# Kernel optimization log

Measured on AMD Instinct MI355X. Metric: run time of the kernel, lower is better.

## Reference

```python
import jax, jax.numpy as jnp
import numpy as np

B, P, ENC, DEC, EMB, ATT, FFN, V, MAXLEN = 64, 196, 512, 512, 256, 128, 1024, 2000, 160
T = MAXLEN - 1
EPS = 1e-5

def _k(i):
    return jax.random.fold_in(jax.random.key(0), i)

def _w(i, shape):
    return jax.random.normal(_k(i), shape, jnp.float32) * 0.02

def setup_inputs() -> dict:
    lens = jnp.concatenate([jnp.array([MAXLEN]), jax.random.randint(_k(2), (B - 1,), 2, MAXLEN + 1)])
    return {
        "encoder_out": jax.random.normal(_k(0), (B, P, ENC), jnp.float32),
        "encoded_captions": jax.random.randint(_k(1), (B, MAXLEN), 0, V),
        "caption_lengths": lens,
        "enc_att_w": _w(3, (ATT, ENC)), "enc_att_b": _w(4, (ATT,)),
        "dec_att_w": _w(5, (ATT, DEC)), "dec_att_b": _w(6, (ATT,)),
        "full_att_w": _w(7, (1, ATT)), "full_att_b": _w(8, (1,)),
        "gate_w1": _w(9, (ATT, DEC)), "gate_b1": _w(10, (ATT,)),
        "gate_w2": _w(11, (1, ATT)), "gate_b2": _w(12, (1,)),
        "emb": jax.random.uniform(_k(13), (V, EMB), jnp.float32, -0.1, 0.1),
        "gru1_wih": _w(14, (3 * DEC, EMB + ENC)), "gru1_whh": _w(15, (3 * DEC, DEC)),
        "gru1_bih": _w(16, (3 * DEC,)), "gru1_bhh": _w(17, (3 * DEC,)),
        "gru2_wih": _w(18, (3 * DEC, DEC)), "gru2_whh": _w(19, (3 * DEC, DEC)),
        "gru2_bih": _w(20, (3 * DEC,)), "gru2_bhh": _w(21, (3 * DEC,)),
        "proj_w": _w(22, (DEC, EMB + ENC)), "proj_b": _w(23, (DEC,)),
        "ln1_g": jnp.ones((DEC,), jnp.float32), "ln1_b": jnp.zeros((DEC,), jnp.float32),
        "ln2_g": jnp.ones((DEC,), jnp.float32), "ln2_b": jnp.zeros((DEC,), jnp.float32),
        "ffn_w1": _w(24, (FFN, DEC)), "ffn_b1": jnp.zeros((FFN,), jnp.float32),
        "ffn_w2": _w(25, (V, FFN)), "ffn_b2": jnp.zeros((V,), jnp.float32),
    }

def _gru(x, h, wih, whh, bih, bhh):
    gi = x @ wih.T + bih
    gh = h @ whh.T + bhh
    ir, iz, ig = jnp.split(gi, 3, axis=-1)
    hr, hz, hg = jnp.split(gh, 3, axis=-1)
    r = jax.nn.sigmoid(ir + hr)
    z = jax.nn.sigmoid(iz + hz)
    n = jnp.tanh(ig + r * hg)
    return (1.0 - z) * n + z * h

def _ln(x, g, b):
    m = x.mean(-1, keepdims=True)
    v = x.var(-1, keepdims=True)
    return (x - m) / jnp.sqrt(v + EPS) * g + b

def _decode(encoder_out, encoded_captions, caption_lengths,
            enc_att_w, enc_att_b, dec_att_w, dec_att_b, full_att_w, full_att_b,
            gate_w1, gate_b1, gate_w2, gate_b2, emb,
            gru1_wih, gru1_whh, gru1_bih, gru1_bhh,
            gru2_wih, gru2_whh, gru2_bih, gru2_bhh,
            proj_w, proj_b, ln1_g, ln1_b, ln2_g, ln2_b,
            ffn_w1, ffn_b1, ffn_w2, ffn_b2):
    # sort by caption length descending (packed-sequence style)
    order = jnp.argsort(-caption_lengths)
    enc = encoder_out[order]                       # [B,P,ENC]
    caps = encoded_captions[order]                 # [B,MAXLEN]
    dec_lens = caption_lengths[order] - 1          # [B]
    att1 = enc @ enc_att_w.T + enc_att_b           # [B,P,ATT] (loop-invariant)
    xs = jnp.swapaxes(emb[caps[:, :T]], 0, 1)      # [T,B,EMB] teacher forcing (p=1.0)
    masks = (jnp.arange(T)[:, None] < dec_lens[None, :]).astype(enc.dtype)  # [T,B]

    def step(carry, inp):
        h1, h2 = carry
        x_t, m = inp                               # [B,EMB], [B]
        att2 = h2 @ dec_att_w.T + dec_att_b        # [B,ATT]
        e = (jax.nn.relu(att1 + att2[:, None, :]) @ full_att_w.T + full_att_b)[..., 0]  # [B,P]
        alpha = jax.nn.softmax(e, axis=1)
        awe = jnp.einsum('bpe,bp->be', enc, alpha)
        gate = jax.nn.sigmoid(jax.nn.relu(h2 @ gate_w1.T + gate_b1) @ gate_w2.T + gate_b2)  # [B,1]
        awe = awe * gate
        gin = jnp.concatenate([x_t, awe], axis=1)  # [B,EMB+ENC]
        h1_new = _gru(gin, h1, gru1_wih, gru1_whh, gru1_bih, gru1_bhh)
        h1_res = _ln(h1_new + gin @ proj_w.T + proj_b, ln1_g, ln1_b)
        h2_new = _gru(h1_res, h2, gru2_wih, gru2_whh, gru2_bih, gru2_bhh)
        h2_res = _ln(h2_new + h1_res, ln2_g, ln2_b)  # dropout is identity (eval)
        preds = jax.nn.relu(h2_res @ ffn_w1.T + ffn_b1) @ ffn_w2.T + ffn_b2  # [B,V]
        mc = m[:, None]
        h1 = jnp.where(mc > 0, h1_new, h1)
        h2 = jnp.where(mc > 0, h2_new, h2)
        return (h1, h2), (preds * mc, alpha * mc)

    h0 = jnp.zeros((enc.shape[0], DEC), enc.dtype)
    _, (preds, alphas) = jax.lax.scan(step, (h0, h0), (xs, masks))
    predictions = jnp.swapaxes(preds, 0, 1)        # [B,T,V]
    alphas = jnp.swapaxes(alphas, 0, 1)            # [B,T,P]
    return predictions, caps, dec_lens, alphas, order

def reference(encoder_out, encoded_captions, caption_lengths,
              enc_att_w, enc_att_b, dec_att_w, dec_att_b, full_att_w, full_att_b,
              gate_w1, gate_b1, gate_w2, gate_b2, emb,
              gru1_wih, gru1_whh, gru1_bih, gru1_bhh,
              gru2_wih, gru2_whh, gru2_bih, gru2_bhh,
              proj_w, proj_b, ln1_g, ln1_b, ln2_g, ln2_b,
              ffn_w1, ffn_b1, ffn_w2, ffn_b2):
    return _decode(encoder_out, encoded_captions, caption_lengths,
                   enc_att_w, enc_att_b, dec_att_w, dec_att_b, full_att_w, full_att_b,
                   gate_w1, gate_b1, gate_w2, gate_b2, emb,
                   gru1_wih, gru1_whh, gru1_bih, gru1_bhh,
                   gru2_wih, gru2_whh, gru2_bih, gru2_bhh,
                   proj_w, proj_b, ln1_g, ln1_b, ln2_g, ln2_b,
                   ffn_w1, ffn_b1, ffn_w2, ffn_b2)
```

## Files before the change

### kernel.cpp

```cpp
#include <hip/hip_runtime.h>
#include <math.h>

#define B 64
#define P 196
#define ENCD 512
#define DECD 512
#define EMBD 256
#define ATTD 128
#define FFND 1024
#define VV 2000
#define MAXLEN 160
#define TSTEPS 159
#define EPS 1e-5f

#define OUT_PRED ((size_t)0)
#define OUT_CAPS ((size_t)(B * TSTEPS * VV))
#define OUT_DECL (OUT_CAPS + (size_t)(B * MAXLEN))
#define OUT_ALPH (OUT_DECL + (size_t)B)
#define OUT_ORDR (OUT_ALPH + (size_t)(B * TSTEPS * P))


struct Ctx {
  const float* enc; const int* caps_in; const int* lens_in;
  const float* eaw; const float* eab; const float* daw; const float* dab;
  const float* faw; const float* fab;
  const float* gw1; const float* gb1; const float* gw2; const float* gb2;
  const float* emb;
  const float* wih1; const float* whh1; const float* bih1; const float* bhh1;
  const float* wih2; const float* whh2; const float* bih2; const float* bhh2;
  const float* projw; const float* projb;
  const float* ln1g; const float* ln1b; const float* ln2g; const float* ln2b;
  const float* fw1; const float* fb1; const float* fw2; const float* fb2;
  int* leafs; int* root;
  int* order_i; int* declen; int* caps_s;
  float* EaT; float* att1;
  float* h1; float* h2; float* v1; float* v2;
  float* gin; float* fgr; float* gh1g; float* gh2g; float* att2acc;
  float* stats1; float* stats2;
  float* WA; float* WB; float* WC; float* WD; float* Watt;
  float* Sf; float* cbf; float* Sg; float* cbg;
  float* out;
};

__device__ __forceinline__ float sigf(float x) { return 1.f / (1.f + __expf(-x)); }

__device__ __forceinline__ float ld4(const float* p) {
  unsigned int u = __hip_atomic_load((const unsigned int*)p, __ATOMIC_RELAXED, __HIP_MEMORY_SCOPE_AGENT);
  return __uint_as_float(u);
}
__device__ __forceinline__ void st4(float* p, float v) {
  __hip_atomic_store((unsigned int*)p, __float_as_uint(v), __ATOMIC_RELAXED, __HIP_MEMORY_SCOPE_AGENT);
}
__device__ __forceinline__ void st8(float* p, float a, float b2) {
  unsigned long long v = ((unsigned long long)__float_as_uint(b2) << 32) | (unsigned long long)__float_as_uint(a);
  __hip_atomic_store((unsigned long long*)p, v, __ATOMIC_RELAXED, __HIP_MEMORY_SCOPE_AGENT);
}
__device__ __forceinline__ void atomF(float* p, float v) {
  __hip_atomic_fetch_add(p, v, __ATOMIC_RELAXED, __HIP_MEMORY_SCOPE_AGENT);
}
__device__ __forceinline__ float4 ldg16(const float* p) {
  float4 d;
  asm volatile("global_load_dwordx4 %0, %1, off sc0 sc1" : "=v"(d) : "v"(p));
  return d;
}
__device__ __forceinline__ void vmwait() { asm volatile("s_waitcnt vmcnt(0)" ::: "memory"); }

__device__ __forceinline__ unsigned short tobf(float x) {
  unsigned int u = __float_as_uint(x);
  u += 0x7fffu + ((u >> 16) & 1u);
  return (unsigned short)(u >> 16);
}
__device__ __forceinline__ float frombf(unsigned short s) {
  return __uint_as_float(((unsigned int)s) << 16);
}


__global__ void k_order(Ctx c) {
  __shared__ int lens[B];
  int tid = threadIdx.x;
  lens[tid] = c.lens_in[tid];
  __syncthreads();
  int li = lens[tid];
  int pos = 0;
  for (int j = 0; j < B; ++j) {
    int lj = lens[j];
    pos += (lj > li || (lj == li && j < tid)) ? 1 : 0;
  }
  c.order_i[pos] = tid;
  c.declen[pos] = li - 1;
  c.out[OUT_ORDR + pos] = (float)tid;
  c.out[OUT_DECL + pos] = (float)(li - 1);
}

__global__ __launch_bounds__(256) void k_caps(Ctx c) {
  int idx = blockIdx.x * 256 + threadIdx.x;
  if (idx < B * MAXLEN) {
    int b = idx / MAXLEN, t = idx - b * MAXLEN;
    int v = c.caps_in[c.order_i[b] * MAXLEN + t];
    c.caps_s[idx] = v;
    c.out[OUT_CAPS + idx] = (float)v;
  }
}

__global__ __launch_bounds__(256) void k_eat(Ctx c) {
  int idx = blockIdx.x * 256 + threadIdx.x;
  if (idx < 128 * 512) {
    int k = idx >> 7, d = idx & 127;
    c.EaT[(size_t)k * 128 + d] = c.eaw[(size_t)d * 512 + k];
  }
}

__global__ __launch_bounds__(256) void k_att1(Ctx c) {
  __shared__ float Xs[8 * 512];
  int tid = threadIdx.x;
  int r0 = blockIdx.x * 8;
  for (int idx = tid; idx < 8 * 512; idx += 256) {
    int rr = idx >> 9, k = idx & 511;
    int r = r0 + rr;
    int b = r / P, p = r - b * P;
    int ob = c.order_i[b];
    Xs[idx] = c.enc[((size_t)(ob * P + p)) * ENCD + k];
  }
  __syncthreads();
  int d = tid >> 1, kh = tid & 1;
  float acc[8];
#pragma unroll
  for (int rr = 0; rr < 8; ++rr) acc[rr] = 0.f;
  int kbase = kh * 256;
  for (int k = 0; k < 256; ++k) {
    float w = c.EaT[(size_t)(kbase + k) * 128 + d];
#pragma unroll
    for (int rr = 0; rr < 8; ++rr) acc[rr] = fmaf(w, Xs[rr * 512 + kbase + k], acc[rr]);
  }
#pragma unroll
  for (int rr = 0; rr < 8; ++rr) {
    acc[rr] += __shfl_xor(acc[rr], 1);
    if (kh == 0) c.att1[(size_t)(r0 + rr) * 128 + d] = acc[rr];
  }
}

__global__ __launch_bounds__(256) void k_wpa(Ctx c) {
  int s = blockIdx.x;
  float* dst = c.WA + (size_t)s * 65536;
  for (int idx = threadIdx.x; idx < 65536; idx += 256) {
    int kb = idx >> 9, r = idx & 511, cc = r >> 2, jj = r & 3;
    int col = s * 128 + cc, k = kb * 4 + jj;
    float v;
    if (col < 1536) v = c.whh1[(size_t)col * 512 + k];
    else if (col < 3072) v = c.whh2[(size_t)(col - 1536) * 512 + k];
    else v = c.ln2g[k] * c.fw1[(size_t)(col - 3072) * 512 + k];
    dst[idx] = v;
  }
}

__global__ __launch_bounds__(256) void k_wpb(Ctx c) {
  int s = blockIdx.x;
  float* dst = c.WB + (size_t)s * 49152;
  for (int idx = threadIdx.x; idx < 49152; idx += 256) {
    int kb = idx >> 8, r = idx & 255, cc = r >> 2, jj = r & 3;
    int u = s * 64 + cc, k = kb * 4 + jj;
    int d = u >> 2, comp = u & 3;
    dst[idx] = (comp < 3) ? c.wih1[(size_t)(comp * 512 + d) * 768 + k]
                          : c.projw[(size_t)d * 768 + k];
  }
}

__global__ __launch_bounds__(256) void k_wpc(Ctx c) {
  int s = blockIdx.x;
  float* dst = c.WC + (size_t)s * 24576;
  for (int idx = threadIdx.x; idx < 24576; idx += 256) {
    int kb = idx / 192, r = idx - kb * 192, cc = r >> 2, jj = r & 3;
    int u = s * 48 + cc, k = kb * 4 + jj;
    int d = u / 3, comp = u - d * 3;
    dst[idx] = c.ln1g[k] * c.wih2[(size_t)(comp * 512 + d) * 512 + k];
  }
}

__global__ __launch_bounds__(256) void k_wpd(Ctx c) {
  int s = blockIdx.x;
  float* dst = c.WD + (size_t)s * 65536;
  for (int idx = threadIdx.x; idx < 65536; idx += 256) {
    int kb = idx >> 8, r = idx & 255, cc = r >> 2, jj = r & 3;
    int vcol = s * 64 + cc, k = kb * 4 + jj;
    dst[idx] = (vcol < 2000) ? c.fw2[(size_t)vcol * 1024 + k] : 0.f;
  }
}

__global__ __launch_bounds__(256) void k_watt(Ctx c) {
  int ks = blockIdx.x;
  float* dst = c.Watt + (size_t)ks * 16384;
  for (int idx = threadIdx.x; idx < 16384; idx += 256) {
    int kb = idx >> 10, r = idx & 1023, cc = r >> 2, jj = r & 3;
    int k = ks * 64 + kb * 4 + jj;
    dst[idx] = (cc < 128) ? c.daw[(size_t)cc * 512 + k] : c.gw1[(size_t)(cc - 128) * 512 + k];
  }
}

__global__ __launch_bounds__(256) void k_consts(Ctx c) {
  __shared__ float r1[256], r2[256];
  int i = blockIdx.x, tid = threadIdx.x;
  float a = 0.f, b2 = 0.f;
  if (i < 1024) {
    const float* w = c.fw1 + (size_t)i * 512;
    for (int k = tid; k < 512; k += 256) { a = fmaf(c.ln2g[k], w[k], a); b2 = fmaf(c.ln2b[k], w[k], b2); }
  } else {
    const float* w = c.wih2 + (size_t)(i - 1024) * 512;
    for (int k = tid; k < 512; k += 256) { a = fmaf(c.ln1g[k], w[k], a); b2 = fmaf(c.ln1b[k], w[k], b2); }
  }
  r1[tid] = a; r2[tid] = b2;
  __syncthreads();
  for (int s = 128; s > 0; s >>= 1) {
    if (tid < s) { r1[tid] += r1[tid + s]; r2[tid] += r2[tid + s]; }
    __syncthreads();
  }
  if (tid == 0) {
    if (i < 1024) { c.Sf[i] = r1[0]; c.cbf[i] = r2[0] + c.fb1[i]; }
    else { c.Sg[i - 1024] = r1[0]; c.cbg[i - 1024] = r2[0] + c.bih2[i - 1024]; }
  }
}


__device__ __forceinline__ void gridbar(int* leafs, int* root, int ph) {
  __builtin_amdgcn_s_waitcnt(0);
  __syncthreads();
  if (threadIdx.x == 0) {
    int old = __hip_atomic_fetch_add(&leafs[(blockIdx.x & 7) * 32], 1,
                                     __ATOMIC_RELAXED, __HIP_MEMORY_SCOPE_AGENT);
    if (old == ph * 32 - 1)
      __hip_atomic_fetch_add(root, 1, __ATOMIC_RELAXED, __HIP_MEMORY_SCOPE_AGENT);
    while (__hip_atomic_load(root, __ATOMIC_RELAXED, __HIP_MEMORY_SCOPE_AGENT) < ph * 8)
      __builtin_amdgcn_s_sleep(1);
  }
  __syncthreads();
}

__global__ __launch_bounds__(512) void persist(Ctx c) {
  __shared__ unsigned short att1L[196 * 130];
  __shared__ unsigned short encL[196 * 128];
  __shared__ float SH[12288];
  __shared__ float eL[256];
  __shared__ float alphaL[256];
  __shared__ float redS[256];
  __shared__ float att2sL[128], fawL[128], dabL[128], gb1L[128];
  __shared__ float sstat[16];
  __shared__ int declenI[64];
  __shared__ float gateL, gb2v, fabv;

  const int g = blockIdx.x;
  const int tid = threadIdx.x;
  const int cg = g & 31;
  const int rg = g >> 5;
  const int r0 = rg * 8;
  const int bA = g >> 2, q = g & 3;
  const int kc = tid >> 6;
  const int ct = tid & 63;

  if (tid < 128) {
    fawL[tid] = c.faw[tid];
    dabL[tid] = c.dab[tid] + c.eab[tid];
    gb1L[tid] = c.gb1[tid];
  }
  if (tid == 0) { gb2v = c.gb2[0]; fabv = c.fab[0]; }
  if (tid < 64) declenI[tid] = c.declen[tid];
  {
    const int ob = c.order_i[bA];
    for (int idx = tid; idx < 196 * 128; idx += 512) {
      int p = idx >> 7, j = idx & 127;
      att1L[p * 130 + j] = tobf(c.att1[((size_t)bA * P + p) * 128 + j]);
      encL[idx] = tobf(c.enc[((size_t)(ob * P + p)) * 512 + q * 128 + j]);
    }
  }
  __syncthreads();

  int ph = 0;
  for (int t = 0; t < MAXLEN; ++t) {
    {
      float* XS = SH;
      float* RED = SH + 4096;
      const float* hsrc = ((cg < 12) ? c.h1 : (cg < 24) ? c.h2 : c.v2) + (size_t)r0 * 512;
      float4 s0 = ldg16(hsrc + tid * 4);
      float4 s1 = ldg16(hsrc + 2048 + tid * 4);
      if (tid < 8) {
        int slot = (t + 1) & 1;
        float a = ld4(c.stats2 + slot * 128 + (r0 + tid) * 2);
        float b2 = ld4(c.stats2 + slot * 128 + (r0 + tid) * 2 + 1);
        float m = a * (1.f / 512.f);
        float va = b2 * (1.f / 512.f) - m * m;
        sstat[tid] = m; sstat[8 + tid] = rsqrtf(va + EPS);
      }
      vmwait();
      *(float4*)(XS + tid * 4) = s0;
      *(float4*)(XS + 2048 + tid * 4) = s1;
      __syncthreads();

      {
        const float* wp = c.WA + (size_t)cg * 65536 + kc * 8192 + ct * 4;
        const float* xb = XS + kc * 64;
        float acc[8][2];
#pragma unroll
        for (int r = 0; r < 8; ++r) { acc[r][0] = 0.f; acc[r][1] = 0.f; }
#pragma unroll 4
        for (int i = 0; i < 16; ++i) {
          float4 w0 = *(const float4*)(wp + i * 512);
          float4 w1 = *(const float4*)(wp + i * 512 + 256);
#pragma unroll
          for (int r = 0; r < 8; ++r) {
            float4 x = *(const float4*)(xb + r * 512 + i * 4);
            acc[r][0] = fmaf(w0.x, x.x, fmaf(w0.y, x.y, fmaf(w0.z, x.z, fmaf(w0.w, x.w, acc[r][0]))));
            acc[r][1] = fmaf(w1.x, x.x, fmaf(w1.y, x.y, fmaf(w1.z, x.z, fmaf(w1.w, x.w, acc[r][1]))));
          }
        }
#pragma unroll
        for (int r = 0; r < 8; ++r) {
          RED[(kc * 8 + r) * 128 + ct] = acc[r][0];
          RED[(kc * 8 + r) * 128 + ct + 64] = acc[r][1];
        }
      }
      if (cg >= 16 && cg < 24) {
        const int ks_att = cg - 16;
        const int ct2 = tid >> 1, half = tid & 1;
        const float* wp = c.Watt + (size_t)ks_att * 16384 + half * 8192 + ct2 * 4;
        const float* xb = XS + ks_att * 64 + half * 32;
        float a[8];
#pragma unroll
        for (int r = 0; r < 8; ++r) a[r] = 0.f;
#pragma unroll
        for (int i = 0; i < 8; ++i) {
          float4 w = *(const float4*)(wp + i * 1024);
#pragma unroll
          for (int r = 0; r < 8; ++r) {
            float4 x = *(const float4*)(xb + r * 512 + i * 4);
            a[r] = fmaf(w.x, x.x, fmaf(w.y, x.y, fmaf(w.z, x.z, fmaf(w.w, x.w, a[r]))));
          }
        }
#pragma unroll
        for (int r = 0; r < 8; ++r) {
          a[r] += __shfl_xor(a[r], 1);
          if (half == 0) atomF(c.att2acc + (r0 + r) * 256 + ct2, a[r]);
        }
      }
      __syncthreads();
      {
        int row = tid >> 6, cp = (tid & 63) * 2;
        float s0_ = 0.f, s1_ = 0.f;
#pragma unroll
        for (int k8 = 0; k8 < 8; ++k8) {
          float2 v = *(const float2*)(RED + (k8 * 8 + row) * 128 + cp);
          s0_ += v.x; s1_ += v.y;
        }
        int bb = r0 + row;
        int gcol = cg * 128 + cp;
        if (cg < 12) st8(c.gh1g + bb * 1536 + gcol, s0_, s1_);
        else if (cg < 24) st8(c.gh2g + bb * 1536 + (gcol - 1536), s0_, s1_);
        else {
          int cf = gcol - 3072;
          float m2 = sstat[row], i2 = sstat[8 + row];
          float v0 = i2 * (s0_ - m2 * c.Sf[cf]) + c.cbf[cf];
          float v1v = i2 * (s1_ - m2 * c.Sf[cf + 1]) + c.cbf[cf + 1];
          st8(c.fgr + bb * 1024 + cf, fmaxf(v0, 0.f), fmaxf(v1v, 0.f));
        }
      }
    }
    gridbar(c.leafs, c.root, ++ph);

    {
      float* XS = SH;
      float* RED = SH + 8192;
      const float* fsrc = c.fgr + (size_t)r0 * 1024;
      float4 s0 = ldg16(fsrc + tid * 4);
      float4 s1 = ldg16(fsrc + 2048 + tid * 4);
      float4 s2 = ldg16(fsrc + 4096 + tid * 4);
      float4 s3 = ldg16(fsrc + 6144 + tid * 4);
      if (g == 0) {
        int sl = t & 1;
        if (tid < 128) st4(c.stats1 + sl * 128 + tid, 0.f);
        else if (tid < 256) st4(c.stats2 + sl * 128 + (tid - 128), 0.f);
      }
      vmwait();
      *(float4*)(XS + tid * 4) = s0;
      *(float4*)(XS + 2048 + tid * 4) = s1;
      *(float4*)(XS + 4096 + tid * 4) = s2;
      *(float4*)(XS + 6144 + tid * 4) = s3;
      __syncthreads();

      {
        const float* wp = c.WD + (size_t)cg * 65536 + kc * 8192 + ct * 4;
        const float* xb = XS + kc * 128;
        float acc[8];
#pragma unroll
        for (int r = 0; r < 8; ++r) acc[r] = 0.f;
#pragma unroll 4
        for (int i = 0; i < 32; ++i) {
          float4 w = *(const float4*)(wp + i * 256);
#pragma unroll
          for (int r = 0; r < 8; ++r) {
            float4 x = *(const float4*)(xb + r * 1024 + i * 4);
            acc[r] = fmaf(w.x, x.x, fmaf(w.y, x.y, fmaf(w.z, x.z, fmaf(w.w, x.w, acc[r]))));
          }
        }
#pragma unroll
        for (int r = 0; r < 8; ++r) RED[(kc * 8 + r) * 64 + ct] = acc[r];
      }
      __syncthreads();
      {
        int row = tid >> 6, cl = tid & 63;
        float s = 0.f;
#pragma unroll
        for (int k8 = 0; k8 < 8; ++k8) s += RED[(k8 * 8 + row) * 64 + cl];
        int bb = r0 + row, vcol = cg * 64 + cl;
        if (vcol < 2000 && t > 0 && (t - 1) < declenI[bb])
          c.out[OUT_PRED + ((size_t)bb * TSTEPS + (t - 1)) * VV + vcol] = s + c.fb2[vcol];
      }
      if (tid < 128) {
        att2sL[tid] = ld4(c.att2acc + bA * 256 + tid) + dabL[tid];
        float g1 = fmaxf(ld4(c.att2acc + bA * 256 + 128 + tid) + gb1L[tid], 0.f);
        redS[tid] = g1 * c.gw2[tid];
      } else if (tid < 256) redS[tid] = 0.f;
      __syncthreads();
      for (int s2_ = 64; s2_ > 0; s2_ >>= 1) {
        if (tid < s2_) redS[tid] += redS[tid + s2_];
        __syncthreads();
      }
      if (tid == 0) gateL = sigf(redS[0] + gb2v);
      __syncthreads();
      {
        int p = tid >> 1, jh = tid & 1;
        float e = 0.f;
        if (p < 196) {
          const unsigned short* ap = att1L + p * 130 + jh * 64;
#pragma unroll 8
          for (int j = 0; j < 64; ++j)
            e = fmaf(fmaxf(frombf(ap[j]) + att2sL[jh * 64 + j], 0.f), fawL[jh * 64 + j], e);
        }
        e += __shfl_xor(e, 1);
        if (jh == 0 && p < 196) eL[p] = e + fabv;
      }
      __syncthreads();
      if (tid < 256) redS[tid] = (tid < 196) ? eL[tid] : -3.0e38f;
      __syncthreads();
      for (int s2_ = 128; s2_ > 0; s2_ >>= 1) {
        if (tid < s2_) redS[tid] = fmaxf(redS[tid], redS[tid + s2_]);
        __syncthreads();
      }
      float mx = redS[0];
      __syncthreads();
      float ex = (tid < 196) ? __expf(eL[tid] - mx) : 0.f;
      if (tid < 256) redS[tid] = ex;
      __syncthreads();
      for (int s2_ = 128; s2_ > 0; s2_ >>= 1) {
        if (tid < s2_) redS[tid] += redS[tid + s2_];
        __syncthreads();
      }
      float inv = 1.f / redS[0];
      if (tid < 256) alphaL[tid] = ex * inv;
      if (q == 0 && tid < 196 && t < declenI[bA])
        c.out[OUT_ALPH + ((size_t)bA * TSTEPS + t) * P + tid] = ex * inv;
      __syncthreads();
      {
        int el = tid & 127, pq = tid >> 7;
        const unsigned short* ep2 = encL + (size_t)(pq * 49) * 128 + el;
        const float* alp = alphaL + pq * 49;
        float s_ = 0.f;
#pragma unroll
        for (int i = 0; i < 49; ++i) s_ = fmaf(alp[i], frombf(ep2[(size_t)i * 128]), s_);
        RED[tid] = s_;
      }
      __syncthreads();
      if (tid < 128) {
        float aw = RED[tid] + RED[128 + tid] + RED[256 + tid] + RED[384 + tid];
        st4(c.gin + bA * 768 + 256 + q * 128 + tid, aw * gateL);
      }
      if (q == 1 && tid < 256) {
        int tok = c.caps_s[bA * MAXLEN + t];
        st4(c.gin + bA * 768 + tid, c.emb[(size_t)tok * 256 + tid]);
      }
    }
    gridbar(c.leafs, c.root, ++ph);

    {
      float* XS = SH;
      float* RED = SH + 6144;
      const float* gsrc = c.gin + (size_t)r0 * 768;
      float4 s0 = ldg16(gsrc + tid * 4);
      float4 s1 = ldg16(gsrc + 2048 + tid * 4);
      float4 s2 = ldg16(gsrc + 4096 + tid * 4);
      if (g < 32) st4(c.att2acc + g * 512 + tid, 0.f);
      vmwait();
      *(float4*)(XS + tid * 4) = s0;
      *(float4*)(XS + 2048 + tid * 4) = s1;
      *(float4*)(XS + 4096 + tid * 4) = s2;
      __syncthreads();

      {
        const float* wp = c.WB + (size_t)cg * 49152 + kc * 6144 + ct * 4;
        const float* xb = XS + kc * 96;
        float acc[8];
#pragma unroll
        for (int r = 0; r < 8; ++r) acc[r] = 0.f;
#pragma unroll 4
        for (int i = 0; i < 24; ++i) {
          float4 w = *(const float4*)(wp + i * 256);
#pragma unroll
          for (int r = 0; r < 8; ++r) {
            float4 x = *(const float4*)(xb + r * 768 + i * 4);
            acc[r] = fmaf(w.x, x.x, fmaf(w.y, x.y, fmaf(w.z, x.z, fmaf(w.w, x.w, acc[r]))));
          }
        }
#pragma unroll
        for (int r = 0; r < 8; ++r) RED[(kc * 8 + r) * 64 + ct] = acc[r];
      }
      __syncthreads();
      if (tid < 128) {
        int row = tid >> 4, dl = tid & 15;
        int bb = r0 + row, d = cg * 16 + dl;
        float gi0 = 0.f, gi1 = 0.f, gi2v = 0.f, gi3 = 0.f;
#pragma unroll
        for (int k8 = 0; k8 < 8; ++k8) {
          float4 v = *(const float4*)(RED + (k8 * 8 + row) * 64 + dl * 4);
          gi0 += v.x; gi1 += v.y; gi2v += v.z; gi3 += v.w;
        }
        float gir = gi0 + c.bih1[d];
        float giz = gi1 + c.bih1[512 + d];
        float gig = gi2v + c.bih1[1024 + d];
        float pj = gi3 + c.projb[d];
        float hr = ld4(c.gh1g + bb * 1536 + d) + c.bhh1[d];
        float hz = ld4(c.gh1g + bb * 1536 + 512 + d) + c.bhh1[512 + d];
        float hg = ld4(c.gh1g + bb * 1536 + 1024 + d) + c.bhh1[1024 + d];
        float r_ = sigf(gir + hr);
        float z_ = sigf(giz + hz);
        float n_ = tanhf(gig + r_ * hg);
        float hold = ld4(c.h1 + bb * 512 + d);
        float hnew = (1.f - z_) * n_ + z_ * hold;
        st4(c.h1 + bb * 512 + d, (t < declenI[bb]) ? hnew : hold);
        float v1v = hnew + pj;
        st4(c.v1 + bb * 512 + d, v1v);
        float ss = v1v, sq = v1v * v1v;
#pragma unroll
        for (int w = 1; w < 16; w <<= 1) { ss += __shfl_xor(ss, w); sq += __shfl_xor(sq, w); }
        if (dl == 0) {
          atomF(c.stats1 + (t & 1) * 128 + bb * 2, ss);
          atomF(c.stats1 + (t & 1) * 128 + bb * 2 + 1, sq);
        }
      }
    }
    gridbar(c.leafs, c.root, ++ph);

    {
      float* XS = SH;
      float* RED = SH + 4096;
      const float* vsrc = c.v1 + (size_t)r0 * 512;
      float4 s0 = ldg16(vsrc + tid * 4);
      float4 s1 = ldg16(vsrc + 2048 + tid * 4);
      if (tid < 8) {
        float a = ld4(c.stats1 + (t & 1) * 128 + (r0 + tid) * 2);
        float b2 = ld4(c.stats1 + (t & 1) * 128 + (r0 + tid) * 2 + 1);
        float m = a * (1.f / 512.f);
        float va = b2 * (1.f / 512.f) - m * m;
        sstat[tid] = m; sstat[8 + tid] = rsqrtf(va + EPS);
      }
      vmwait();
      *(float4*)(XS + tid * 4) = s0;
      *(float4*)(XS + 2048 + tid * 4) = s1;
      __syncthreads();

      if (ct < 48) {
        const float* wp = c.WC + (size_t)cg * 24576 + kc * 3072 + ct * 4;
        const float* xb = XS + kc * 64;
        float acc[8];
#pragma unroll
        for (int r = 0; r < 8; ++r) acc[r] = 0.f;
#pragma unroll 4
        for (int i = 0; i < 16; ++i) {
          float4 w = *(const float4*)(wp + i * 192);
#pragma unroll
          for (int r = 0; r < 8; ++r) {
            float4 x = *(const float4*)(xb + r * 512 + i * 4);
            acc[r] = fmaf(w.x, x.x, fmaf(w.y, x.y, fmaf(w.z, x.z, fmaf(w.w, x.w, acc[r]))));
          }
        }
#pragma unroll
        for (int r = 0; r < 8; ++r) RED[(kc * 8 + r) * 48 + ct] = acc[r];
      }
      __syncthreads();
      if (tid < 128) {
        int row = tid >> 4, dl = tid & 15;
        int bb = r0 + row, d = cg * 16 + dl;
        float gi0 = 0.f, gi1 = 0.f, gi2v = 0.f;
#pragma unroll
        for (int k8 = 0; k8 < 8; ++k8) {
          const float* rp = RED + (k8 * 8 + row) * 48 + dl * 3;
          gi0 += rp[0]; gi1 += rp[1]; gi2v += rp[2];
        }
        float m1 = sstat[row], i1 = sstat[8 + row];
        float gir = i1 * (gi0 - m1 * c.Sg[d]) + c.cbg[d];
        float giz = i1 * (gi1 - m1 * c.Sg[512 + d]) + c.cbg[512 + d];
        float gig = i1 * (gi2v - m1 * c.Sg[1024 + d]) + c.cbg[1024 + d];
        float hr = ld4(c.gh2g + bb * 1536 + d) + c.bhh2[d];
        float hz = ld4(c.gh2g + bb * 1536 + 512 + d) + c.bhh2[512 + d];
        float hg = ld4(c.gh2g + bb * 1536 + 1024 + d) + c.bhh2[1024 + d];
        float r_ = sigf(gir + hr);
        float z_ = sigf(giz + hz);
        float n_ = tanhf(gig + r_ * hg);
        float hold = ld4(c.h2 + bb * 512 + d);
        float hnew = (1.f - z_) * n_ + z_ * hold;
        st4(c.h2 + bb * 512 + d, (t < declenI[bb]) ? hnew : hold);
        float h1r = (XS[row * 512 + d] - m1) * i1 * c.ln1g[d] + c.ln1b[d];
        float v2v = hnew + h1r;
        st4(c.v2 + bb * 512 + d, v2v);
        float ss = v2v, sq = v2v * v2v;
#pragma unroll
        for (int w = 1; w < 16; w <<= 1) { ss += __shfl_xor(ss, w); sq += __shfl_xor(sq, w); }
        if (dl == 0) {
          atomF(c.stats2 + (t & 1) * 128 + bb * 2, ss);
          atomF(c.stats2 + (t & 1) * 128 + bb * 2 + 1, sq);
        }
      }
    }
    gridbar(c.leafs, c.root, ++ph);
  }
}

extern "C" void kernel_launch(void* const* d_in, const int* in_sizes, int n_in,
                              void* d_out, int out_size, void* d_ws, size_t ws_size,
                              hipStream_t stream) {
  (void)in_sizes; (void)n_in; (void)ws_size;
  Ctx c;
  c.enc = (const float*)d_in[0];
  c.caps_in = (const int*)d_in[1];
  c.lens_in = (const int*)d_in[2];
  c.eaw = (const float*)d_in[3];
  c.eab = (const float*)d_in[4];
  c.daw = (const float*)d_in[5];
  c.dab = (const float*)d_in[6];
  c.faw = (const float*)d_in[7];
  c.fab = (const float*)d_in[8];
  c.gw1 = (const float*)d_in[9];
  c.gb1 = (const float*)d_in[10];
  c.gw2 = (const float*)d_in[11];
  c.gb2 = (const float*)d_in[12];
  c.emb = (const float*)d_in[13];
  c.wih1 = (const float*)d_in[14];
  c.whh1 = (const float*)d_in[15];
  c.bih1 = (const float*)d_in[16];
  c.bhh1 = (const float*)d_in[17];
  c.wih2 = (const float*)d_in[18];
  c.whh2 = (const float*)d_in[19];
  c.bih2 = (const float*)d_in[20];
  c.bhh2 = (const float*)d_in[21];
  c.projw = (const float*)d_in[22];
  c.projb = (const float*)d_in[23];
  c.ln1g = (const float*)d_in[24];
  c.ln1b = (const float*)d_in[25];
  c.ln2g = (const float*)d_in[26];
  c.ln2b = (const float*)d_in[27];
  c.fw1 = (const float*)d_in[28];
  c.fb1 = (const float*)d_in[29];
  c.fw2 = (const float*)d_in[30];
  c.fb2 = (const float*)d_in[31];
  c.out = (float*)d_out;

  char* wp_ = (char*)d_ws;
  auto alloc = [&](size_t bytes) -> char* {
    char* p = wp_;
    wp_ += (bytes + 255) & ~(size_t)255;
    return p;
  };
  char* zbase = wp_;
  c.leafs = (int*)alloc(256 * 4);
  c.root = (int*)alloc(256);
  c.h1 = (float*)alloc((size_t)B * 512 * 4);
  c.h2 = (float*)alloc((size_t)B * 512 * 4);
  c.stats1 = (float*)alloc(2 * 64 * 2 * 4);
  c.stats2 = (float*)alloc(2 * 64 * 2 * 4);
  c.att2acc = (float*)alloc((size_t)B * 256 * 4);
  c.v2 = (float*)alloc((size_t)B * 512 * 4);
  size_t zbytes = (size_t)(wp_ - zbase);

  c.order_i = (int*)alloc(B * 4);
  c.declen = (int*)alloc(B * 4);
  c.caps_s = (int*)alloc((size_t)B * MAXLEN * 4);
  c.EaT = (float*)alloc((size_t)512 * 128 * 4);
  c.att1 = (float*)alloc((size_t)B * P * 128 * 4);
  c.v1 = (float*)alloc((size_t)B * 512 * 4);
  c.gin = (float*)alloc((size_t)B * 768 * 4);
  c.fgr = (float*)alloc((size_t)B * 1024 * 4);
  c.gh1g = (float*)alloc((size_t)B * 1536 * 4);
  c.gh2g = (float*)alloc((size_t)B * 1536 * 4);
  c.WA = (float*)alloc((size_t)32 * 65536 * 4);
  c.WB = (float*)alloc((size_t)32 * 49152 * 4);
  c.WC = (float*)alloc((size_t)32 * 24576 * 4);
  c.WD = (float*)alloc((size_t)32 * 65536 * 4);
  c.Watt = (float*)alloc((size_t)8 * 16384 * 4);
  c.Sf = (float*)alloc(1024 * 4);
  c.cbf = (float*)alloc(1024 * 4);
  c.Sg = (float*)alloc(1536 * 4);
  c.cbg = (float*)alloc(1536 * 4);

  hipMemsetAsync(d_out, 0, (size_t)out_size * 4, stream);
  hipMemsetAsync(zbase, 0, zbytes, stream);

  k_order<<<1, 64, 0, stream>>>(c);
  k_caps<<<(B * MAXLEN + 255) / 256, 256, 0, stream>>>(c);
  k_eat<<<(128 * 512 + 255) / 256, 256, 0, stream>>>(c);
  k_att1<<<(B * P) / 8, 256, 0, stream>>>(c);
  k_wpa<<<32, 256, 0, stream>>>(c);
  k_wpb<<<32, 256, 0, stream>>>(c);
  k_wpc<<<32, 256, 0, stream>>>(c);
  k_wpd<<<32, 256, 0, stream>>>(c);
  k_watt<<<8, 256, 0, stream>>>(c);
  k_consts<<<2560, 256, 0, stream>>>(c);

  persist<<<256, 512, 0, stream>>>(c);
}
```

Measured before the change: 13.97 ms.

## Prefetch next-phase weights before grid barriers and use wave-shuffle reductions

At the end of each phase of the persistent kernel, each thread issues dummy global loads covering the weight slice the next phase will read. The intent is to warm L2/MALL during the grid barrier so the next GEMV does not stall on cold weight fetches. It also replaces the tree-based shared-memory reductions for the gate, softmax max and softmax sum with wave-level shuffle reductions, cutting many __syncthreads. The gate inputs are now loaded early, alongside the fgr loads. The cost is extra memory traffic and register pressure, and the sink asm forces each phase to wait for the prefetch loads to complete.

Result: slower. 14.38 ms (+3.0%).

```diff
diff --git a/kernel.cpp b/kernel.cpp
--- a/kernel.cpp
+++ b/kernel.cpp
@@ -65,6 +65,19 @@
 }
 __device__ __forceinline__ void vmwait() { asm volatile("s_waitcnt vmcnt(0)" ::: "memory"); }
 
+__device__ __forceinline__ float pfl(const float* p) {
+  float v;
+  asm volatile("global_load_dword %0, %1, off" : "=v"(v) : "v"(p));
+  return v;
+}
+__device__ __forceinline__ void pfsink8(float a, float b, float c2, float d,
+                                        float e, float f, float g2, float h) {
+  asm volatile("" :: "v"(a), "v"(b), "v"(c2), "v"(d), "v"(e), "v"(f), "v"(g2), "v"(h));
+}
+__device__ __forceinline__ void pfsink2(float a, float b) {
+  asm volatile("" :: "v"(a), "v"(b));
+}
+
 __device__ __forceinline__ unsigned short tobf(float x) {
   unsigned int u = __float_as_uint(x);
   u += 0x7fffu + ((u >> 16) & 1u);
@@ -240,11 +253,11 @@
   __shared__ float SH[12288];
   __shared__ float eL[256];
   __shared__ float alphaL[256];
-  __shared__ float redS[256];
-  __shared__ float att2sL[128], fawL[128], dabL[128], gb1L[128];
+  __shared__ float att2sL[128], fawL[128], dabL[128], gb1L[128], gw2L[128];
+  __shared__ float wred[16];
   __shared__ float sstat[16];
   __shared__ int declenI[64];
-  __shared__ float gateL, gb2v, fabv;
+  __shared__ float gb2v, fabv;
 
   const int g = blockIdx.x;
   const int tid = threadIdx.x;
@@ -259,6 +272,7 @@
     fawL[tid] = c.faw[tid];
     dabL[tid] = c.dab[tid] + c.eab[tid];
     gb1L[tid] = c.gb1[tid];
+    gw2L[tid] = c.gw2[tid];
   }
   if (tid == 0) { gb2v = c.gb2[0]; fabv = c.fab[0]; }
   if (tid < 64) declenI[tid] = c.declen[tid];
@@ -339,6 +353,12 @@
           if (half == 0) atomF(c.att2acc + (r0 + r) * 256 + ct2, a[r]);
         }
       }
+      float pw[8];
+      {
+        const float* pb = c.WD + (size_t)cg * 65536 + tid * 16;
+#pragma unroll
+        for (int i = 0; i < 8; ++i) pw[i] = pfl(pb + i * 8192);
+      }
       __syncthreads();
       {
         int row = tid >> 6, cp = (tid & 63) * 2;
@@ -360,6 +380,7 @@
           st8(c.fgr + bb * 1024 + cf, fmaxf(v0, 0.f), fmaxf(v1v, 0.f));
         }
       }
+      pfsink8(pw[0], pw[1], pw[2], pw[3], pw[4], pw[5], pw[6], pw[7]);
     }
     gridbar(c.leafs, c.root, ++ph);
 
@@ -371,6 +392,11 @@
       float4 s1 = ldg16(fsrc + 2048 + tid * 4);
       float4 s2 = ldg16(fsrc + 4096 + tid * 4);
       float4 s3 = ldg16(fsrc + 6144 + tid * 4);
+      float a2r = 0.f, g1r = 0.f;
+      if (tid < 128) {
+        a2r = ld4(c.att2acc + bA * 256 + tid);
+        g1r = ld4(c.att2acc + bA * 256 + 128 + tid);
+      }
       if (g == 0) {
         int sl = t & 1;
         if (tid < 128) st4(c.stats1 + sl * 128 + tid, 0.f);
@@ -381,6 +407,14 @@
       *(float4*)(XS + 2048 + tid * 4) = s1;
       *(float4*)(XS + 4096 + tid * 4) = s2;
       *(float4*)(XS + 6144 + tid * 4) = s3;
+      if (tid < 128) {
+        att2sL[tid] = a2r + dabL[tid];
+        float g1 = fmaxf(g1r + gb1L[tid], 0.f);
+        float gv = g1 * gw2L[tid];
+#pragma unroll
+        for (int w = 1; w < 64; w <<= 1) gv += __shfl_xor(gv, w);
+        if ((tid & 63) == 0) wred[tid >> 6] = gv;
+      }
       __syncthreads();
 
       {
@@ -401,6 +435,12 @@
 #pragma unroll
         for (int r = 0; r < 8; ++r) RED[(kc * 8 + r) * 64 + ct] = acc[r];
       }
+      float pw[6];
+      {
+        const float* pb = c.WB + (size_t)cg * 49152 + tid * 16;
+#pragma unroll
+        for (int i = 0; i < 6; ++i) pw[i] = pfl(pb + i * 8192);
+      }
       __syncthreads();
       {
         int row = tid >> 6, cl = tid & 63;
@@ -411,18 +451,6 @@
         if (vcol < 2000 && t > 0 && (t - 1) < declenI[bb])
           c.out[OUT_PRED + ((size_t)bb * TSTEPS + (t - 1)) * VV + vcol] = s + c.fb2[vcol];
       }
-      if (tid < 128) {
-        att2sL[tid] = ld4(c.att2acc + bA * 256 + tid) + dabL[tid];
-        float g1 = fmaxf(ld4(c.att2acc + bA * 256 + 128 + tid) + gb1L[tid], 0.f);
-        redS[tid] = g1 * c.gw2[tid];
-      } else if (tid < 256) redS[tid] = 0.f;
-      __syncthreads();
-      for (int s2_ = 64; s2_ > 0; s2_ >>= 1) {
-        if (tid < s2_) redS[tid] += redS[tid + s2_];
-        __syncthreads();
-      }
-      if (tid == 0) gateL = sigf(redS[0] + gb2v);
-      __syncthreads();
       {
         int p = tid >> 1, jh = tid & 1;
         float e = 0.f;
@@ -436,22 +464,25 @@
         if (jh == 0 && p < 196) eL[p] = e + fabv;
       }
       __syncthreads();
-      if (tid < 256) redS[tid] = (tid < 196) ? eL[tid] : -3.0e38f;
-      __syncthreads();
-      for (int s2_ = 128; s2_ > 0; s2_ >>= 1) {
-        if (tid < s2_) redS[tid] = fmaxf(redS[tid], redS[tid + s2_]);
-        __syncthreads();
-      }
-      float mx = redS[0];
-      __syncthreads();
-      float ex = (tid < 196) ? __expf(eL[tid] - mx) : 0.f;
-      if (tid < 256) redS[tid] = ex;
-      __syncthreads();
-      for (int s2_ = 128; s2_ > 0; s2_ >>= 1) {
-        if (tid < s2_) redS[tid] += redS[tid + s2_];
-        __syncthreads();
-      }
-      float inv = 1.f / redS[0];
+      float ev = (tid < 196) ? eL[tid] : -3.0e38f;
+      if (tid < 256) {
+        float mv = ev;
+#pragma unroll
+        for (int w = 1; w < 64; w <<= 1) mv = fmaxf(mv, __shfl_xor(mv, w));
+        if ((tid & 63) == 0) wred[2 + (tid >> 6)] = mv;
+      }
+      __syncthreads();
+      float mx = fmaxf(fmaxf(wred[2], wred[3]), fmaxf(wred[4], wred[5]));
+      float ex = (tid < 196) ? __expf(ev - mx) : 0.f;
+      if (tid < 256) {
+        float sv = ex;
+#pragma unroll
+        for (int w = 1; w < 64; w <<= 1) sv += __shfl_xor(sv, w);
+        if ((tid & 63) == 0) wred[6 + (tid >> 6)] = sv;
+      }
+      __syncthreads();
+      float inv = 1.f / (wred[6] + wred[7] + wred[8] + wred[9]);
+      float gate = sigf(wred[0] + wred[1] + gb2v);
       if (tid < 256) alphaL[tid] = ex * inv;
       if (q == 0 && tid < 196 && t < declenI[bA])
         c.out[OUT_ALPH + ((size_t)bA * TSTEPS + t) * P + tid] = ex * inv;
@@ -468,12 +499,13 @@
       __syncthreads();
       if (tid < 128) {
         float aw = RED[tid] + RED[128 + tid] + RED[256 + tid] + RED[384 + tid];
-        st4(c.gin + bA * 768 + 256 + q * 128 + tid, aw * gateL);
+        st4(c.gin + bA * 768 + 256 + q * 128 + tid, aw * gate);
       }
       if (q == 1 && tid < 256) {
         int tok = c.caps_s[bA * MAXLEN + t];
         st4(c.gin + bA * 768 + tid, c.emb[(size_t)tok * 256 + tid]);
       }
+      pfsink8(pw[0], pw[1], pw[2], pw[3], pw[4], pw[5], pw[0], pw[1]);
     }
     gridbar(c.leafs, c.root, ++ph);
 
@@ -508,6 +540,12 @@
         }
 #pragma unroll
         for (int r = 0; r < 8; ++r) RED[(kc * 8 + r) * 64 + ct] = acc[r];
+      }
+      float pw[3];
+      {
+        const float* pb = c.WC + (size_t)cg * 24576 + tid * 16;
+#pragma unroll
+        for (int i = 0; i < 3; ++i) pw[i] = pfl(pb + i * 8192);
       }
       __syncthreads();
       if (tid < 128) {
@@ -542,6 +580,7 @@
           atomF(c.stats1 + (t & 1) * 128 + bb * 2 + 1, sq);
         }
       }
+      pfsink8(pw[0], pw[1], pw[2], pw[0], pw[1], pw[2], pw[0], pw[1]);
     }
     gridbar(c.leafs, c.root, ++ph);
 
@@ -580,6 +619,18 @@
         }
 #pragma unroll
         for (int r = 0; r < 8; ++r) RED[(kc * 8 + r) * 48 + ct] = acc[r];
+      }
+      float pw[8];
+      {
+        const float* pb = c.WA + (size_t)cg * 65536 + tid * 16;
+#pragma unroll
+        for (int i = 0; i < 8; ++i) pw[i] = pfl(pb + i * 8192);
+      }
+      float pa0 = 0.f, pa1 = 0.f;
+      if (cg >= 16 && cg < 24) {
+        const float* pb = c.Watt + (size_t)(cg - 16) * 16384 + tid * 16;
+        pa0 = pfl(pb);
+        pa1 = pfl(pb + 8192);
       }
       __syncthreads();
       if (tid < 128) {
@@ -615,6 +666,8 @@
           atomF(c.stats2 + (t & 1) * 128 + bb * 2 + 1, sq);
         }
       }
+      pfsink8(pw[0], pw[1], pw[2], pw[3], pw[4], pw[5], pw[6], pw[7]);
+      pfsink2(pa0, pa1);
     }
     gridbar(c.leafs, c.root, ++ph);
   }
```
